# Kernel optimization log

Hardware: AMD Instinct MI355X
Metric: run time of the kernel (lower is better)

The kernel has to match this reference:

```python
import jax, jax.numpy as jnp
import numpy as np

V = 32000      # vocab size
D = 256        # embedding_dim
HOPS = 3       # max_hops
MAXS = 1024    # max_s (positional table has MAXS+1 rows)
PAD = 0        # pad_id


def _pos_table(n_position, d):
    pos = np.arange(n_position)[:, None].astype(np.float64)
    j = np.arange(d)[None, :]
    angle = pos / np.power(10000.0, 2 * (j // 2) / d)
    tab = angle.copy()
    tab[1:, 0::2] = np.sin(angle[1:, 0::2])
    tab[1:, 1::2] = np.cos(angle[1:, 1::2])
    tab[0] = 0.0
    return jnp.asarray(tab, dtype=jnp.float32)


def setup_inputs() -> dict:
    key = jax.random.key(0)
    ks = jax.random.split(key, 10)
    M, B, T = 1024, 32, 4
    story = jax.random.randint(ks[0], (M, B, T), 0, V, dtype=jnp.int64)
    enc_query = jax.random.randint(ks[1], (B,), 0, V, dtype=jnp.int64)
    last_hidden = jax.random.normal(ks[2], (1, B, D), dtype=jnp.float32)
    # C_0..C_HOPS embedding tables, N(0, 0.1), pad row zeroed (padding_idx)
    C = 0.1 * jax.random.normal(ks[3], (HOPS + 1, V, D), dtype=jnp.float32)
    C = C.at[:, PAD].set(0.0)
    pos_table = _pos_table(MAXS + 1, D)
    W1_w = 0.02 * jax.random.normal(ks[4], (V, 2 * D), dtype=jnp.float32)
    W1_b = jnp.zeros((V,), dtype=jnp.float32)
    gru_w_ih = 0.05 * jax.random.normal(ks[5], (3 * D, D), dtype=jnp.float32)
    gru_w_hh = 0.05 * jax.random.normal(ks[6], (3 * D, D), dtype=jnp.float32)
    gru_b_ih = 0.05 * jax.random.normal(ks[7], (3 * D,), dtype=jnp.float32)
    gru_b_hh = 0.05 * jax.random.normal(ks[8], (3 * D,), dtype=jnp.float32)
    return {"story": story, "enc_query": enc_query, "last_hidden": last_hidden,
            "C": C, "pos_table": pos_table, "W1_w": W1_w, "W1_b": W1_b,
            "gru_w_ih": gru_w_ih, "gru_w_hh": gru_w_hh,
            "gru_b_ih": gru_b_ih, "gru_b_hh": gru_b_hh}


def _gru_step(x, h, w_ih, w_hh, b_ih, b_hh):
    # single-step torch.nn.GRU cell math; x,h: [B, D]
    gi = x @ w_ih.T + b_ih
    gh = h @ w_hh.T + b_hh
    i_r, i_z, i_n = jnp.split(gi, 3, axis=-1)
    h_r, h_z, h_n = jnp.split(gh, 3, axis=-1)
    r = jax.nn.sigmoid(i_r + h_r)
    z = jax.nn.sigmoid(i_z + h_z)
    n = jnp.tanh(i_n + r * h_n)
    return (1.0 - z) * n + z * h


def reference(story, enc_query, last_hidden, C, pos_table, W1_w, W1_b,
              gru_w_ih, gru_w_hh, gru_b_ih, gru_b_hh):
    # --- load_memory ---
    s = jnp.transpose(story, (1, 0, 2))            # [B, M, T]
    pad_mask = s[:, :, 0] == PAD                   # [B, M]
    positions = jnp.cumsum((~pad_mask).astype(jnp.int32), axis=-1)
    positions = jnp.where(pad_mask, 0, positions)
    embed_pos = pos_table[positions]               # [B, M, D]
    m_story = []
    for hop in range(HOPS + 1):
        m_A = C[hop][s].sum(axis=2)                # gather [B,M,T,D] -> sum over T
        if hop == 0:
            m_A = m_A + embed_pos
        m_story.append(m_A)
    # --- ptrMemDecoder ---
    embed_q = C[0][enc_query]                      # [B, D]
    h_new = _gru_step(embed_q, last_hidden[0], gru_w_ih, gru_w_hh, gru_b_ih, gru_b_hh)
    hidden = h_new[None]                           # [1, B, D]
    u = h_new
    u0 = h_new
    p_vocab = None
    prob_lg = None
    for hop in range(HOPS):
        m_A = m_story[hop]
        prob_lg = jnp.einsum('bmd,bd->bm', m_A, u)
        prob = jax.nn.softmax(prob_lg, axis=1)
        m_C = m_story[hop + 1]
        o_k = jnp.einsum('bm,bmd->bd', prob, m_C)
        if hop == 0:
            p_vocab = jnp.concatenate([u0, o_k], axis=1) @ W1_w.T + W1_b
        u = u + o_k
    return prob_lg, p_vocab, hidden
```

## Files before the change

kernel.cpp:

```cpp
#include <hip/hip_runtime.h>
#include <hip/hip_bf16.h>

#define VSZ 32000
#define DSZ 256
#define BSZ 32
#define MSZ 1024
#define PSZ 1025
#define VD  (VSZ * DSZ)
#define XBP 264

#define OFF_U     32768
#define OFF_U0    40960
#define OFF_PP    49152
#define OFF_GIH   81952
#define OFF_SC    131104
#define OFF_PMAX  163872
#define OFF_PSUM  167968
#define OFF_PROJ  172064

#define OUT_PV  (BSZ * MSZ)
#define OUT_HID (OUT_PV + BSZ * VSZ)

typedef __attribute__((ext_vector_type(8))) short bfrag;
typedef __attribute__((ext_vector_type(4))) float f32x4;

__device__ __forceinline__ short bfc(float f) {
    __hip_bfloat16 h = __float2bfloat16(f);
    return __builtin_bit_cast(short, h);
}

__device__ __forceinline__ bfrag cvt8(float4 a, float4 b) {
    bfrag f;
    f[0] = bfc(a.x); f[1] = bfc(a.y); f[2] = bfc(a.z); f[3] = bfc(a.w);
    f[4] = bfc(b.x); f[5] = bfc(b.y); f[6] = bfc(b.z); f[7] = bfc(b.w);
    return f;
}

__device__ __forceinline__ void stage_xb(const float* __restrict__ src,
                                         short* __restrict__ xB, int t) {
    for (int i = t; i < BSZ * 64; i += 256) {
        int b = i >> 6, c4 = i & 63;
        float4 v = ((const float4*)src)[i];
        short4 pk = make_short4(bfc(v.x), bfc(v.y), bfc(v.z), bfc(v.w));
        *(short4*)&xB[(size_t)b * XBP + c4 * 4] = pk;
    }
}

__device__ __forceinline__ void stage_xb_diff(const float* __restrict__ a,
                                              const float* __restrict__ c,
                                              short* __restrict__ xB, int t) {
    for (int i = t; i < BSZ * 64; i += 256) {
        int b = i >> 6, c4 = i & 63;
        float4 va = ((const float4*)a)[i];
        float4 vc = ((const float4*)c)[i];
        short4 pk = make_short4(bfc(va.x - vc.x), bfc(va.y - vc.y),
                                bfc(va.z - vc.z), bfc(va.w - vc.w));
        *(short4*)&xB[(size_t)b * XBP + c4 * 4] = pk;
    }
}

__device__ __forceinline__ void mfma_direct(
    const float* __restrict__ W, int wstride, int rbeg, int nrows,
    const short* __restrict__ xB, f32x4 (&acc)[4][2], int t)
{
    const int lane = t & 63, w = t >> 6;
    const int m = lane & 15, kg = lane >> 4;
    bfrag xb[8][2];
#pragma unroll
    for (int kc = 0; kc < 8; ++kc) {
        xb[kc][0] = *(const bfrag*)&xB[(size_t)m * XBP + kc * 32 + kg * 8];
        xb[kc][1] = *(const bfrag*)&xB[(size_t)(16 + m) * XBP + kc * 32 + kg * 8];
    }
    const float* wp[4];
#pragma unroll
    for (int rt = 0; rt < 4; ++rt) {
        int r = w * 64 + rt * 16 + m;
        int rc = (r < nrows) ? r : 0;
        wp[rt] = W + (size_t)(rbeg + rc) * wstride + kg * 8;
    }
    float4 cur[4][2], nxt[4][2];
#pragma unroll
    for (int rt = 0; rt < 4; ++rt) {
        cur[rt][0] = *(const float4*)(wp[rt]);
        cur[rt][1] = *(const float4*)(wp[rt] + 4);
    }
    for (int kt = 0; kt < 8; ++kt) {
        if (kt < 7) {
#pragma unroll
            for (int rt = 0; rt < 4; ++rt) {
                nxt[rt][0] = *(const float4*)(wp[rt] + (kt + 1) * 32);
                nxt[rt][1] = *(const float4*)(wp[rt] + (kt + 1) * 32 + 4);
            }
        }
#pragma unroll
        for (int rt = 0; rt < 4; ++rt) {
            bfrag af = cvt8(cur[rt][0], cur[rt][1]);
            acc[rt][0] = __builtin_amdgcn_mfma_f32_16x16x32_bf16(af, xb[kt][0], acc[rt][0], 0, 0, 0);
            acc[rt][1] = __builtin_amdgcn_mfma_f32_16x16x32_bf16(af, xb[kt][1], acc[rt][1], 0, 0, 0);
        }
#pragma unroll
        for (int rt = 0; rt < 4; ++rt) { cur[rt][0] = nxt[rt][0]; cur[rt][1] = nxt[rt][1]; }
    }
}

__device__ __forceinline__ void mfma_store(
    const f32x4 (&acc)[4][2], float* __restrict__ dest,
    const float* __restrict__ bias, size_t drow, size_t dcol,
    int rbeg, int nrows, int t)
{
    const int lane = t & 63, w = t >> 6;
    const int n = lane & 15, rq = lane >> 4;
#pragma unroll
    for (int rt = 0; rt < 4; ++rt) {
#pragma unroll
        for (int g = 0; g < 4; ++g) {
            int r = w * 64 + rt * 16 + rq * 4 + g;
            if (r < nrows) {
                float bv = bias ? bias[rbeg + r] : 0.f;
                dest[(size_t)(rbeg + r) * drow + (size_t)n * dcol] = acc[rt][0][g] + bv;
                dest[(size_t)(rbeg + r) * drow + (size_t)(16 + n) * dcol] = acc[rt][1][g] + bv;
            }
        }
    }
}

__device__ __forceinline__ void acc_zero(f32x4 (&acc)[4][2]) {
#pragma unroll
    for (int rt = 0; rt < 4; ++rt)
#pragma unroll
        for (int bt = 0; bt < 2; ++bt) {
            f32x4 z = {0.f, 0.f, 0.f, 0.f};
            acc[rt][bt] = z;
        }
}

__global__ __launch_bounds__(256) void k_posgru(
    const int* __restrict__ story, const int* __restrict__ encq,
    const float* __restrict__ lasth, const float* __restrict__ C0,
    const float* __restrict__ gwih, const float* __restrict__ gwhh,
    int* __restrict__ pos, float* __restrict__ gih)
{
    __shared__ short xB[32 * XBP];
    __shared__ int wtot[4];
    int gid = blockIdx.x, t = threadIdx.x;
    int lane = t & 63, wid = t >> 6;
    if (gid < 32) {
        int b = gid, m0 = t * 4;
        int f0 = story[(size_t)((m0 + 0) * BSZ + b) * 4] != 0;
        int f1 = story[(size_t)((m0 + 1) * BSZ + b) * 4] != 0;
        int f2 = story[(size_t)((m0 + 2) * BSZ + b) * 4] != 0;
        int f3 = story[(size_t)((m0 + 3) * BSZ + b) * 4] != 0;
        int p1 = f0 + f1, p2 = p1 + f2, p3 = p2 + f3;
        int x = p3;
        for (int o = 1; o < 64; o <<= 1) {
            int v = __shfl_up(x, o, 64);
            if (lane >= o) x += v;
        }
        if (lane == 63) wtot[wid] = x;
        __syncthreads();
        int wo = 0;
        for (int i = 0; i < wid; ++i) wo += wtot[i];
        int base = wo + x - p3;
        pos[(m0 + 0) * BSZ + b] = f0 ? base + f0 : 0;
        pos[(m0 + 1) * BSZ + b] = f1 ? base + p1 : 0;
        pos[(m0 + 2) * BSZ + b] = f2 ? base + p2 : 0;
        pos[(m0 + 3) * BSZ + b] = f3 ? base + p3 : 0;
    } else {
        int k = gid - 32;
        bool isX = (k < 3);
        for (int i = t; i < BSZ * 64; i += 256) {
            int b = i >> 6, c4 = i & 63;
            float4 v = isX ? ((const float4*)(C0 + (size_t)encq[b] * DSZ))[c4]
                           : ((const float4*)(lasth + (size_t)b * DSZ))[c4];
            short4 pk = make_short4(bfc(v.x), bfc(v.y), bfc(v.z), bfc(v.w));
            *(short4*)&xB[(size_t)b * XBP + c4 * 4] = pk;
        }
        __syncthreads();
        int kr = isX ? k : k - 3;
        const float* W = isX ? gwih : gwhh;
        float* dest = gih + (isX ? 0 : 768 * BSZ);
        f32x4 acc[4][2];
        acc_zero(acc);
        mfma_direct(W, DSZ, kr * 256, 256, xB, acc, t);
        mfma_store(acc, dest, nullptr, BSZ, 1, kr * 256, 256, t);
    }
}

__global__ void k_grufin(const float* __restrict__ gih,
                         const float* __restrict__ gbih, const float* __restrict__ gbhh,
                         const float* __restrict__ lasth,
                         float* __restrict__ u, float* __restrict__ u0,
                         float* __restrict__ hid)
{
    int idx = blockIdx.x * 256 + threadIdx.x;
    int b = idx & 31, d = idx >> 5;
    float gi0 = gih[(size_t)(0 * DSZ + d) * BSZ + b] + gbih[0 * DSZ + d];
    float gi1 = gih[(size_t)(1 * DSZ + d) * BSZ + b] + gbih[1 * DSZ + d];
    float gi2 = gih[(size_t)(2 * DSZ + d) * BSZ + b] + gbih[2 * DSZ + d];
    float gh0 = gih[(size_t)(3 * DSZ + d) * BSZ + b] + gbhh[0 * DSZ + d];
    float gh1 = gih[(size_t)(4 * DSZ + d) * BSZ + b] + gbhh[1 * DSZ + d];
    float gh2 = gih[(size_t)(5 * DSZ + d) * BSZ + b] + gbhh[2 * DSZ + d];
    float r = 1.f / (1.f + __expf(-(gi0 + gh0)));
    float z = 1.f / (1.f + __expf(-(gi1 + gh1)));
    float n = tanhf(gi2 + r * gh2);
    float h = lasth[(size_t)b * DSZ + d];
    float hn = (1.f - z) * n + z * h;
    int o = b * DSZ + d;
    u[o] = hn; u0[o] = hn; hid[o] = hn;
}

__global__ __launch_bounds__(256) void k_proj(
    const float* __restrict__ Ct, const float* __restrict__ postab,
    const float* __restrict__ u, float* __restrict__ proj,
    float* __restrict__ pp, int nproj)
{
    __shared__ short xB[32 * XBP];
    int gid = blockIdx.x, t = threadIdx.x;
    stage_xb(u, xB, t);
    __syncthreads();
    f32x4 acc[4][2];
    acc_zero(acc);
    if (gid < nproj) {
        int rb = gid * 256;
        mfma_direct(Ct, DSZ, rb, 256, xB, acc, t);
        mfma_store(acc, proj, nullptr, 1, VSZ, rb, 256, t);
    } else {
        int rb = (gid - nproj) * 256;
        int nr = min(256, PSZ - rb);
        mfma_direct(postab, DSZ, rb, nr, xB, acc, t);
        mfma_store(acc, pp, nullptr, 1, PSZ, rb, nr, t);
    }
}

__global__ void k_scores(const int* __restrict__ story, const int* __restrict__ pos,
                         const float* __restrict__ proj, const float* __restrict__ pp,
                         float* __restrict__ sc, float* __restrict__ pmax,
                         float* __restrict__ psum, float* __restrict__ outlg, int hop)
{
    __shared__ float red[256];
    int gid = blockIdx.x, t = threadIdx.x;
    int idx = gid * 256 + t;
    int b = idx & 31, m = idx >> 5;
    int4 st = *(const int4*)&story[(size_t)idx * 4];
    const float* pb = proj + (size_t)b * VSZ;
    float s = pb[st.x] + pb[st.y] + pb[st.z] + pb[st.w];
    if (hop == 0) s += pp[(size_t)b * PSZ + pos[idx]];
    if (hop == 2) { outlg[b * MSZ + m] = s; return; }
    sc[idx] = s;
    red[t] = s;
    __syncthreads();
    if (t < 32) {
        float mx = red[t];
#pragma unroll
        for (int k = 1; k < 8; ++k) mx = fmaxf(mx, red[k * 32 + t]);
        float sm = 0.f;
#pragma unroll
        for (int k = 0; k < 8; ++k) sm += __expf(red[k * 32 + t] - mx);
        pmax[gid * 32 + t] = mx;
        psum[gid * 32 + t] = sm;
    }
}

__global__ __launch_bounds__(256) void k_okpv(
    const int* __restrict__ story, const float* __restrict__ sc,
    const float* __restrict__ pmax, const float* __restrict__ psum,
    const float* __restrict__ Ct, float* __restrict__ u)
{
    int b = blockIdx.x & 31, mc = blockIdx.x >> 5;
    int t = threadIdx.x;
    __shared__ float red[256];
    __shared__ float pl[32];
    __shared__ float4 pt[4][64];
    red[t] = (t < 128) ? pmax[t * 32 + b] : -3.4e38f;
    __syncthreads();
    for (int o = 128; o >= 1; o >>= 1) {
        if (t < o) red[t] = fmaxf(red[t], red[t + o]);
        __syncthreads();
    }
    float M = red[0];
    __syncthreads();
    red[t] = (t < 128) ? psum[t * 32 + b] * __expf(pmax[t * 32 + b] - M) : 0.f;
    __syncthreads();
    for (int o = 128; o >= 1; o >>= 1) {
        if (t < o) red[t] += red[t + o];
        __syncthreads();
    }
    float S = red[0];
    __syncthreads();
    if (t < 32) pl[t] = __expf(sc[(size_t)(mc * 32 + t) * BSZ + b] - M) / S;
    __syncthreads();
    int dl = t & 63, mg = t >> 6;
    int mbase = mc * 32 + mg * 8;
    float4 acc = make_float4(0.f, 0.f, 0.f, 0.f);
    int4 st = *(const int4*)&story[(size_t)(mbase * BSZ + b) * 4];
    float pw = pl[mg * 8];
#pragma unroll
    for (int i = 0; i < 8; ++i) {
        int4 s_ = st; float p_ = pw;
        if (i < 7) {
            st = *(const int4*)&story[(size_t)((mbase + i + 1) * BSZ + b) * 4];
            pw = pl[mg * 8 + i + 1];
        }
        float4 a0 = ((const float4*)(Ct + (size_t)s_.x * DSZ))[dl];
        float4 a1 = ((const float4*)(Ct + (size_t)s_.y * DSZ))[dl];
        float4 a2 = ((const float4*)(Ct + (size_t)s_.z * DSZ))[dl];
        float4 a3 = ((const float4*)(Ct + (size_t)s_.w * DSZ))[dl];
        acc.x += p_ * (a0.x + a1.x + a2.x + a3.x);
        acc.y += p_ * (a0.y + a1.y + a2.y + a3.y);
        acc.z += p_ * (a0.z + a1.z + a2.z + a3.z);
        acc.w += p_ * (a0.w + a1.w + a2.w + a3.w);
    }
    pt[mg][dl] = acc;
    __syncthreads();
    if (t < 64) {
        float4 s0 = pt[0][t], s1 = pt[1][t], s2 = pt[2][t], s3 = pt[3][t];
        float* dst = &u[(size_t)b * DSZ + t * 4];
        atomicAdd(dst + 0, s0.x + s1.x + s2.x + s3.x);
        atomicAdd(dst + 1, s0.y + s1.y + s2.y + s3.y);
        atomicAdd(dst + 2, s0.z + s1.z + s2.z + s3.z);
        atomicAdd(dst + 3, s0.w + s1.w + s2.w + s3.w);
    }
}

__global__ __launch_bounds__(256) void k_tail0(
    const float* __restrict__ C1, const float* __restrict__ u,
    const float* __restrict__ u0, const float* __restrict__ W1w,
    const float* __restrict__ W1b, float* __restrict__ proj,
    float* __restrict__ out_pv)
{
    __shared__ short xB[32 * XBP];
    int gid = blockIdx.x, t = threadIdx.x;
    f32x4 acc[4][2];
    acc_zero(acc);
    if (gid < 125) {
        int rb = gid * 256;
        stage_xb(u0, xB, t);
        __syncthreads();
        mfma_direct(W1w, 512, rb, 256, xB, acc, t);
        __syncthreads();
        stage_xb_diff(u, u0, xB, t);
        __syncthreads();
        mfma_direct(W1w + 256, 512, rb, 256, xB, acc, t);
        mfma_store(acc, out_pv, W1b, 1, VSZ, rb, 256, t);
    } else {
        stage_xb(u, xB, t);
        __syncthreads();
        int rb = (gid - 125) * 256;
        mfma_direct(C1, DSZ, rb, 256, xB, acc, t);
        mfma_store(acc, proj, nullptr, 1, VSZ, rb, 256, t);
    }
}

extern "C" void kernel_launch(void* const* d_in, const int* in_sizes, int n_in,
                              void* d_out, int out_size, void* d_ws, size_t ws_size,
                              hipStream_t stream) {
    const int*   story  = (const int*)d_in[0];
    const int*   encq   = (const int*)d_in[1];
    const float* lasth  = (const float*)d_in[2];
    const float* C      = (const float*)d_in[3];
    const float* postab = (const float*)d_in[4];
    const float* W1w    = (const float*)d_in[5];
    const float* W1b    = (const float*)d_in[6];
    const float* gwih   = (const float*)d_in[7];
    const float* gwhh   = (const float*)d_in[8];
    const float* gbih   = (const float*)d_in[9];
    const float* gbhh   = (const float*)d_in[10];

    float* out = (float*)d_out;
    float* wsf = (float*)d_ws;
    int*   pos  = (int*)d_ws;
    float* u    = wsf + OFF_U;
    float* u0   = wsf + OFF_U0;
    float* pp   = wsf + OFF_PP;
    float* gih  = wsf + OFF_GIH;
    float* sc   = wsf + OFF_SC;
    float* pmax = wsf + OFF_PMAX;
    float* psum = wsf + OFF_PSUM;
    float* proj = wsf + OFF_PROJ;

    k_posgru<<<38, 256, 0, stream>>>(story, encq, lasth, C, gwih, gwhh, pos, gih);
    k_grufin<<<32, 256, 0, stream>>>(gih, gbih, gbhh, lasth, u, u0, out + OUT_HID);
    k_proj<<<130, 256, 0, stream>>>(C, postab, u, proj, pp, 125);

    for (int hop = 0; hop < 3; ++hop) {
        k_scores<<<128, 256, 0, stream>>>(story, pos, proj, pp, sc, pmax, psum,
                                          out, hop);
        if (hop == 2) break;
        k_okpv<<<1024, 256, 0, stream>>>(story, sc, pmax, psum,
                                         C + (size_t)(hop + 1) * VD, u);
        if (hop == 0) {
            k_tail0<<<250, 256, 0, stream>>>(C + (size_t)VD, u, u0, W1w, W1b,
                                             proj, out + OUT_PV);
        } else {
            k_proj<<<125, 256, 0, stream>>>(C + (size_t)2 * VD, nullptr, u, proj,
                                            nullptr, 125);
        }
    }
}
```

Before: 134.9 us.

## Halve rows per block and deepen weight prefetch to four stages in MFMA GEMVs

```diff
diff --git a/kernel.cpp b/kernel.cpp
--- a/kernel.cpp
+++ b/kernel.cpp
@@ -59,9 +59,10 @@
     }
 }
 
-__device__ __forceinline__ void mfma_direct(
+template <int NRT>
+__device__ __forceinline__ void mfma_deep(
     const float* __restrict__ W, int wstride, int rbeg, int nrows,
-    const short* __restrict__ xB, f32x4 (&acc)[4][2], int t)
+    const short* __restrict__ xB, f32x4 (&acc)[NRT][2], int t)
 {
     const int lane = t & 63, w = t >> 6;
     const int m = lane & 15, kg = lane >> 4;
@@ -71,50 +72,53 @@
         xb[kc][0] = *(const bfrag*)&xB[(size_t)m * XBP + kc * 32 + kg * 8];
         xb[kc][1] = *(const bfrag*)&xB[(size_t)(16 + m) * XBP + kc * 32 + kg * 8];
     }
-    const float* wp[4];
-#pragma unroll
-    for (int rt = 0; rt < 4; ++rt) {
-        int r = w * 64 + rt * 16 + m;
+    const float* wp[NRT];
+#pragma unroll
+    for (int rt = 0; rt < NRT; ++rt) {
+        int r = w * (NRT * 16) + rt * 16 + m;
         int rc = (r < nrows) ? r : 0;
         wp[rt] = W + (size_t)(rbeg + rc) * wstride + kg * 8;
     }
-    float4 cur[4][2], nxt[4][2];
-#pragma unroll
-    for (int rt = 0; rt < 4; ++rt) {
-        cur[rt][0] = *(const float4*)(wp[rt]);
-        cur[rt][1] = *(const float4*)(wp[rt] + 4);
-    }
+    float4 wbuf[4][NRT][2];
+#pragma unroll
+    for (int p = 0; p < 4; ++p)
+#pragma unroll
+        for (int rt = 0; rt < NRT; ++rt) {
+            wbuf[p][rt][0] = *(const float4*)(wp[rt] + p * 32);
+            wbuf[p][rt][1] = *(const float4*)(wp[rt] + p * 32 + 4);
+        }
+#pragma unroll
     for (int kt = 0; kt < 8; ++kt) {
-        if (kt < 7) {
-#pragma unroll
-            for (int rt = 0; rt < 4; ++rt) {
-                nxt[rt][0] = *(const float4*)(wp[rt] + (kt + 1) * 32);
-                nxt[rt][1] = *(const float4*)(wp[rt] + (kt + 1) * 32 + 4);
-            }
-        }
-#pragma unroll
-        for (int rt = 0; rt < 4; ++rt) {
-            bfrag af = cvt8(cur[rt][0], cur[rt][1]);
+        const int s = kt & 3;
+#pragma unroll
+        for (int rt = 0; rt < NRT; ++rt) {
+            bfrag af = cvt8(wbuf[s][rt][0], wbuf[s][rt][1]);
             acc[rt][0] = __builtin_amdgcn_mfma_f32_16x16x32_bf16(af, xb[kt][0], acc[rt][0], 0, 0, 0);
             acc[rt][1] = __builtin_amdgcn_mfma_f32_16x16x32_bf16(af, xb[kt][1], acc[rt][1], 0, 0, 0);
         }
-#pragma unroll
-        for (int rt = 0; rt < 4; ++rt) { cur[rt][0] = nxt[rt][0]; cur[rt][1] = nxt[rt][1]; }
-    }
-}
-
+        if (kt < 4) {
+#pragma unroll
+            for (int rt = 0; rt < NRT; ++rt) {
+                wbuf[s][rt][0] = *(const float4*)(wp[rt] + (kt + 4) * 32);
+                wbuf[s][rt][1] = *(const float4*)(wp[rt] + (kt + 4) * 32 + 4);
+            }
+        }
+    }
+}
+
+template <int NRT>
 __device__ __forceinline__ void mfma_store(
-    const f32x4 (&acc)[4][2], float* __restrict__ dest,
+    const f32x4 (&acc)[NRT][2], float* __restrict__ dest,
     const float* __restrict__ bias, size_t drow, size_t dcol,
     int rbeg, int nrows, int t)
 {
     const int lane = t & 63, w = t >> 6;
     const int n = lane & 15, rq = lane >> 4;
 #pragma unroll
-    for (int rt = 0; rt < 4; ++rt) {
+    for (int rt = 0; rt < NRT; ++rt) {
 #pragma unroll
         for (int g = 0; g < 4; ++g) {
-            int r = w * 64 + rt * 16 + rq * 4 + g;
+            int r = w * (NRT * 16) + rt * 16 + rq * 4 + g;
             if (r < nrows) {
                 float bv = bias ? bias[rbeg + r] : 0.f;
                 dest[(size_t)(rbeg + r) * drow + (size_t)n * dcol] = acc[rt][0][g] + bv;
@@ -124,9 +128,10 @@
     }
 }
 
-__device__ __forceinline__ void acc_zero(f32x4 (&acc)[4][2]) {
-#pragma unroll
-    for (int rt = 0; rt < 4; ++rt)
+template <int NRT>
+__device__ __forceinline__ void acc_zero(f32x4 (&acc)[NRT][2]) {
+#pragma unroll
+    for (int rt = 0; rt < NRT; ++rt)
 #pragma unroll
         for (int bt = 0; bt < 2; ++bt) {
             f32x4 z = {0.f, 0.f, 0.f, 0.f};
@@ -134,7 +139,7 @@
         }
 }
 
-__global__ __launch_bounds__(256) void k_posgru(
+__global__ __launch_bounds__(256, 1) void k_posgru(
     const int* __restrict__ story, const int* __restrict__ encq,
     const float* __restrict__ lasth, const float* __restrict__ C0,
     const float* __restrict__ gwih, const float* __restrict__ gwhh,
@@ -167,7 +172,7 @@
         pos[(m0 + 3) * BSZ + b] = f3 ? base + p3 : 0;
     } else {
         int k = gid - 32;
-        bool isX = (k < 3);
+        bool isX = (k < 6);
         for (int i = t; i < BSZ * 64; i += 256) {
             int b = i >> 6, c4 = i & 63;
             float4 v = isX ? ((const float4*)(C0 + (size_t)encq[b] * DSZ))[c4]
@@ -176,13 +181,13 @@
             *(short4*)&xB[(size_t)b * XBP + c4 * 4] = pk;
         }
         __syncthreads();
-        int kr = isX ? k : k - 3;
+        int kr = isX ? k : k - 6;
         const float* W = isX ? gwih : gwhh;
         float* dest = gih + (isX ? 0 : 768 * BSZ);
-        f32x4 acc[4][2];
-        acc_zero(acc);
-        mfma_direct(W, DSZ, kr * 256, 256, xB, acc, t);
-        mfma_store(acc, dest, nullptr, BSZ, 1, kr * 256, 256, t);
+        f32x4 acc[2][2];
+        acc_zero<2>(acc);
+        mfma_deep<2>(W, DSZ, kr * 128, 128, xB, acc, t);
+        mfma_store<2>(acc, dest, nullptr, BSZ, 1, kr * 128, 128, t);
     }
 }
 
@@ -209,7 +214,7 @@
     u[o] = hn; u0[o] = hn; hid[o] = hn;
 }
 
-__global__ __launch_bounds__(256) void k_proj(
+__global__ __launch_bounds__(256, 1) void k_proj(
     const float* __restrict__ Ct, const float* __restrict__ postab,
     const float* __restrict__ u, float* __restrict__ proj,
     float* __restrict__ pp, int nproj)
@@ -218,17 +223,17 @@
     int gid = blockIdx.x, t = threadIdx.x;
     stage_xb(u, xB, t);
     __syncthreads();
-    f32x4 acc[4][2];
-    acc_zero(acc);
+    f32x4 acc[2][2];
+    acc_zero<2>(acc);
     if (gid < nproj) {
-        int rb = gid * 256;
-        mfma_direct(Ct, DSZ, rb, 256, xB, acc, t);
-        mfma_store(acc, proj, nullptr, 1, VSZ, rb, 256, t);
+        int rb = gid * 128;
+        mfma_deep<2>(Ct, DSZ, rb, 128, xB, acc, t);
+        mfma_store<2>(acc, proj, nullptr, 1, VSZ, rb, 128, t);
     } else {
-        int rb = (gid - nproj) * 256;
-        int nr = min(256, PSZ - rb);
-        mfma_direct(postab, DSZ, rb, nr, xB, acc, t);
-        mfma_store(acc, pp, nullptr, 1, PSZ, rb, nr, t);
+        int rb = (gid - nproj) * 128;
+        int nr = min(128, PSZ - rb);
+        mfma_deep<2>(postab, DSZ, rb, nr, xB, acc, t);
+        mfma_store<2>(acc, pp, nullptr, 1, PSZ, rb, nr, t);
     }
 }
 
@@ -322,7 +327,7 @@
     }
 }
 
-__global__ __launch_bounds__(256) void k_tail0(
+__global__ __launch_bounds__(256, 1) void k_tail0(
     const float* __restrict__ C1, const float* __restrict__ u,
     const float* __restrict__ u0, const float* __restrict__ W1w,
     const float* __restrict__ W1b, float* __restrict__ proj,
@@ -330,24 +335,24 @@
 {
     __shared__ short xB[32 * XBP];
     int gid = blockIdx.x, t = threadIdx.x;
-    f32x4 acc[4][2];
-    acc_zero(acc);
-    if (gid < 125) {
-        int rb = gid * 256;
+    f32x4 acc[2][2];
+    acc_zero<2>(acc);
+    if (gid < 250) {
+        int rb = gid * 128;
         stage_xb(u0, xB, t);
         __syncthreads();
-        mfma_direct(W1w, 512, rb, 256, xB, acc, t);
+        mfma_deep<2>(W1w, 512, rb, 128, xB, acc, t);
         __syncthreads();
         stage_xb_diff(u, u0, xB, t);
         __syncthreads();
-        mfma_direct(W1w + 256, 512, rb, 256, xB, acc, t);
-        mfma_store(acc, out_pv, W1b, 1, VSZ, rb, 256, t);
+        mfma_deep<2>(W1w + 256, 512, rb, 128, xB, acc, t);
+        mfma_store<2>(acc, out_pv, W1b, 1, VSZ, rb, 128, t);
     } else {
         stage_xb(u, xB, t);
         __syncthreads();
-        int rb = (gid - 125) * 256;
-        mfma_direct(C1, DSZ, rb, 256, xB, acc, t);
-        mfma_store(acc, proj, nullptr, 1, VSZ, rb, 256, t);
+        int rb = (gid - 250) * 128;
+        mfma_deep<2>(C1, DSZ, rb, 128, xB, acc, t);
+        mfma_store<2>(acc, proj, nullptr, 1, VSZ, rb, 128, t);
     }
 }
 
@@ -378,9 +383,9 @@
     float* psum = wsf + OFF_PSUM;
     float* proj = wsf + OFF_PROJ;
 
-    k_posgru<<<38, 256, 0, stream>>>(story, encq, lasth, C, gwih, gwhh, pos, gih);
+    k_posgru<<<44, 256, 0, stream>>>(story, encq, lasth, C, gwih, gwhh, pos, gih);
     k_grufin<<<32, 256, 0, stream>>>(gih, gbih, gbhh, lasth, u, u0, out + OUT_HID);
-    k_proj<<<130, 256, 0, stream>>>(C, postab, u, proj, pp, 125);
+    k_proj<<<259, 256, 0, stream>>>(C, postab, u, proj, pp, 250);
 
     for (int hop = 0; hop < 3; ++hop) {
         k_scores<<<128, 256, 0, stream>>>(story, pos, proj, pp, sc, pmax, psum,
@@ -389,11 +394,11 @@
         k_okpv<<<1024, 256, 0, stream>>>(story, sc, pmax, psum,
                                          C + (size_t)(hop + 1) * VD, u);
         if (hop == 0) {
-            k_tail0<<<250, 256, 0, stream>>>(C + (size_t)VD, u, u0, W1w, W1b,
+            k_tail0<<<500, 256, 0, stream>>>(C + (size_t)VD, u, u0, W1w, W1b,
                                              proj, out + OUT_PV);
         } else {
-            k_proj<<<125, 256, 0, stream>>>(C + (size_t)2 * VD, nullptr, u, proj,
-                                            nullptr, 125);
-        }
-    }
-}
+            k_proj<<<250, 256, 0, stream>>>(C + (size_t)2 * VD, nullptr, u, proj,
+                                            nullptr, 250);
+        }
+    }
+}
```

New measurement: 121.6 us. 1.11x faster.
